# Optimization experiments

Hardware: AMD Instinct MI355X
Metric: run time of the kernel (lower is better)

The kernel has to match this reference:

```python
import jax, jax.numpy as jnp
import numpy as np

B, T, D = 16, 1024, 256   # batch, tokens, embedding_dim
Q, K = 4, 4096            # num_quantizers, n_embed
BETA = 1.0


def l2norm(x, eps=1e-12):
    n = jnp.linalg.norm(x, axis=-1, keepdims=True)
    return x / jnp.maximum(n, eps)


def vq_stage(z, codebook):
    """NormEMAVectorQuantizer forward (eval math; EMA buffer update omitted).
    z: (B,T,D) float; codebook: (K,D) l2-normalized rows.
    Returns straight-through quantized (B,T,D), scalar commit loss, indices (N,).
    """
    zn = l2norm(z)                                   # normalize input features
    zf = zn.reshape(-1, zn.shape[-1])                # (N, D)
    # squared euclidean distances (N, K): |z|^2 + |e|^2 - 2 z.e
    d = (jnp.sum(zf * zf, axis=1, keepdims=True)
         + jnp.sum(codebook * codebook, axis=1)[None, :]
         - 2.0 * zf @ codebook.T)
    idx = jnp.argmin(d, axis=1)                      # (N,)
    z_q = codebook[idx].reshape(zn.shape)            # gather codewords
    loss = BETA * jnp.mean((jax.lax.stop_gradient(z_q) - zn) ** 2)
    z_q = zn + jax.lax.stop_gradient(z_q - zn)       # straight-through
    return z_q, loss, idx


def setup_inputs() -> dict:
    key = jax.random.key(0)
    kx, kc = jax.random.split(key)
    x = jax.random.normal(kx, (B, T, D), dtype=jnp.float32)
    # EMA codebooks are kept l2-normalized in NormEMAVectorQuantizer
    codebooks = l2norm(jax.random.normal(kc, (Q, K, D), dtype=jnp.float32))
    return {"x": x, "codebooks": codebooks}


def reference(x, codebooks):
    residual = x
    quantized_outputs, losses, indices = [], [], []
    for q in range(codebooks.shape[0]):              # fixed small stage count
        z_q, loss, idx = vq_stage(residual, codebooks[q])
        # faithful to source: value of residual is unchanged, gradient path added
        residual = residual - jax.lax.stop_gradient(z_q) + z_q
        quantized_outputs.append(z_q)
        losses.append(loss)
        indices.append(idx)
    quantized_sum = quantized_outputs[0]
    for t in quantized_outputs[1:]:
        quantized_sum = quantized_sum + t
    total_loss = losses[0]
    for l in losses[1:]:
        total_loss = total_loss + l
    return quantized_sum, total_loss, jnp.stack(indices, axis=1)  # (N, Q) int
```

## Files before the change

### kernel.cpp

```cpp
#include <hip/hip_runtime.h>
#include <stdint.h>


#define NR 16384
#define DIM 256
#define KCB 4096
#define QST 4
#define MARGIN_DOT 4e-4f
#define MARGIN2_DOT 2e-5f
#define CAPL 4096

typedef _Float16 f16;
typedef __attribute__((ext_vector_type(4))) f16 f16x4;
typedef __attribute__((ext_vector_type(8))) f16 f16x8;
typedef __attribute__((ext_vector_type(4))) float f32x4;

#define WS_ZN_HI   ((size_t)0)
#define WS_ZN_LO   ((size_t)8*1024*1024)
#define WS_CB_HI   ((size_t)16*1024*1024)
#define WS_CB_LO   ((size_t)24*1024*1024)
#define WS_NORMS   ((size_t)32*1024*1024)
#define WS_SSQ     (WS_NORMS + 65536)
#define WS_TOPS    (WS_SSQ + 65536)
#define WS_IDX     (WS_TOPS + (size_t)QST*NR*2*16)
#define WS_LIST    (WS_IDX + (size_t)QST*NR*4)
#define WS_LIST2   (WS_LIST + (size_t)QST*CAPL*4)
#define WS_TOPS2   (WS_LIST2 + (size_t)QST*NR*4)
#define WS_CNT     (WS_TOPS2 + (size_t)QST*CAPL*16*16)
#define WS_PART    (WS_CNT + 64)
#define WS_TOPS3   (WS_PART + 16384)

__device__ __forceinline__ void gll16(const void* g, void* l) {
  __builtin_amdgcn_global_load_lds(
      (const __attribute__((address_space(1))) void*)g,
      (__attribute__((address_space(3))) void*)l, 16, 0, 0);
}

__device__ __forceinline__ float dot4chain(const float4* __restrict__ c,
                                           const float4* __restrict__ z) {
  float dot = 0.f;
  for (int d = 0; d < 64; ++d) {
    const float4 cv = c[d], zv = z[d];
    dot += cv.x * zv.x + cv.y * zv.y + cv.z * zv.z + cv.w * zv.w;
  }
  return dot;
}

__global__ void prep_kernel(const float* __restrict__ x, const float* __restrict__ cb,
                            char* __restrict__ ws) {
  const int w = threadIdx.x >> 6, lane = threadIdx.x & 63;
  const int normalize = (blockIdx.x < (NR / 4));
  const int blk = normalize ? blockIdx.x : blockIdx.x - (NR / 4);
  const float* src = normalize ? x : cb;
  const int row = blk * 4 + w;
  const float4 v = ((const float4*)src)[row * 64 + lane];
  float ss = v.x * v.x + v.y * v.y + v.z * v.z + v.w * v.w;
#pragma unroll
  for (int m = 32; m; m >>= 1) ss += __shfl_xor(ss, m);
  float4 z = v;
  f16 *hi, *lo;
  if (normalize) {
    const float denom = fmaxf(sqrtf(ss), 1e-12f);
    z.x = v.x / denom; z.y = v.y / denom; z.z = v.z / denom; z.w = v.w / denom;
    hi = (f16*)(ws + WS_ZN_HI); lo = (f16*)(ws + WS_ZN_LO);
    if (lane == 0) ((float*)(ws + WS_NORMS))[row] = denom;
    if (blockIdx.x == 0 && threadIdx.x < 8) ((int*)(ws + WS_CNT))[threadIdx.x] = 0;
  } else {
    hi = (f16*)(ws + WS_CB_HI); lo = (f16*)(ws + WS_CB_LO);
    if (lane == 0) ((float*)(ws + WS_SSQ))[row] = ss;
  }
  f16x4 h, l;
  h[0] = (f16)z.x; h[1] = (f16)z.y; h[2] = (f16)z.z; h[3] = (f16)z.w;
  l[0] = (f16)(z.x - (float)h[0]); l[1] = (f16)(z.y - (float)h[1]);
  l[2] = (f16)(z.z - (float)h[2]); l[3] = (f16)(z.w - (float)h[3]);
  ((f16x4*)hi)[row * 64 + lane] = h;
  ((f16x4*)lo)[row * 64 + lane] = l;
}

__launch_bounds__(256, 2)
__global__ void score_kernel(char* __restrict__ ws) {
  __shared__ __align__(16) f16 A0[128][64];
  __shared__ __align__(16) f16 A1[128][64];
  __shared__ __align__(16) f16 B0[128][64];
  __shared__ __align__(16) f16 B1[128][64];
  const int tid = threadIdx.x, w = tid >> 6, lane = tid & 63;
  const int wr = w >> 1, wc = w & 1;
  const int blk = blockIdx.x;
  const int xcd = blk & 7, st = xcd >> 1;
  const int rowtile = ((xcd & 1) << 6) + (blk >> 3);
  const int rowBase = rowtile << 7;

  const f16* zn_hi = (const f16*)(ws + WS_ZN_HI);
  const f16* cb_hi = (const f16*)(ws + WS_CB_HI);

  const int reg = w >> 1;
  const int half = w & 1;
  const int g0 = (lane & 7) ^ ((lane >> 3) & 7);
  const size_t laneOff = (size_t)(lane >> 3) * DIM + (size_t)g0 * 8;
  const f16* srcA0 = zn_hi + (size_t)(rowBase + half * 64) * DIM + laneOff;
  const f16* srcB0 = cb_hi + ((size_t)st * KCB + half * 64) * DIM + laneOff;

  f16* dst0 = reg ? &B0[half * 64][0] : &A0[half * 64][0];
  f16* dst1 = reg ? &B1[half * 64][0] : &A1[half * 64][0];

  float t1[16], t2[16]; int i1[16];
#pragma unroll
  for (int s = 0; s < 16; ++s) { t1[s] = -3.4e38f; t2[s] = -3.4e38f; i1[s] = 0; }
  const int colLane = wc * 64 + (lane & 15);

  auto SRC = [&](int ct, int dc) -> const f16* {
    return reg ? (srcB0 + (size_t)ct * 128 * DIM + dc * 64) : (srcA0 + dc * 64);
  };
  auto STAGE = [&](f16* dst, const f16* sp) {
#pragma unroll
    for (int op = 0; op < 8; ++op)
      gll16(sp + op * 8 * DIM, dst + op * 512);
  };

  f32x4 acc[4][4];
  const f32x4 zero4 = {0.f, 0.f, 0.f, 0.f};

  auto PHASE = [&](const f16* As, const f16* Bs, f16* stDst, const f16* stSrc,
                   bool doStage, bool init) {
    f16x8 ah[2][4], bh[2][4];
#pragma unroll
    for (int kk = 0; kk < 2; ++kk) {
#pragma unroll
      for (int m = 0; m < 4; ++m) {
        const int rl = wr * 64 + m * 16 + (lane & 15);
        const int slot = ((kk << 2) + (lane >> 4)) ^ (rl & 7);
        ah[kk][m] = *(const f16x8*)(As + rl * 64 + slot * 8);
      }
#pragma unroll
      for (int n = 0; n < 4; ++n) {
        const int cl = wc * 64 + n * 16 + (lane & 15);
        const int slot = ((kk << 2) + (lane >> 4)) ^ (cl & 7);
        bh[kk][n] = *(const f16x8*)(Bs + cl * 64 + slot * 8);
      }
    }
    if (doStage) STAGE(stDst, stSrc);
#pragma unroll
    for (int kk = 0; kk < 2; ++kk)
#pragma unroll
      for (int n = 0; n < 4; ++n) {
        if (init && kk == 0) {
#pragma unroll
          for (int m = 0; m < 4; ++m)
            acc[m][n] = __builtin_amdgcn_mfma_f32_16x16x32_f16(ah[0][m], bh[0][n], zero4, 0, 0, 0);
        } else {
#pragma unroll
          for (int m = 0; m < 4; ++m)
            acc[m][n] = __builtin_amdgcn_mfma_f32_16x16x32_f16(ah[kk][m], bh[kk][n], acc[m][n], 0, 0, 0);
        }
      }
    __syncthreads();
  };

  STAGE(dst0, SRC(0, 0));
  __syncthreads();

  for (int ct = 0; ct < 32; ++ct) {
    PHASE(&A0[0][0], &B0[0][0], dst1, SRC(ct, 1), true, true);
    PHASE(&A1[0][0], &B1[0][0], dst0, SRC(ct, 2), true, false);
    PHASE(&A0[0][0], &B0[0][0], dst1, SRC(ct, 3), true, false);
    PHASE(&A1[0][0], &B1[0][0], dst0, SRC(ct + 1, 0), ct < 31, false);
#pragma unroll
    for (int n = 0; n < 4; ++n) {
      const int col = ct * 128 + n * 16 + colLane;
#pragma unroll
      for (int m = 0; m < 4; ++m)
#pragma unroll
        for (int rr = 0; rr < 4; ++rr) {
          const float sc = acc[m][n][rr];
          const int sl = m * 4 + rr;
          if (sc > t1[sl]) { t2[sl] = t1[sl]; t1[sl] = sc; i1[sl] = col; }
          else t2[sl] = fmaxf(t2[sl], sc);
        }
    }
  }

  float* mv1 = (float*)&A0[0][0];
  float* mv2 = mv1 + 256;
  int*   mi1v = (int*)(mv2 + 256);
#pragma unroll
  for (int m = 0; m < 4; ++m)
#pragma unroll
    for (int rr = 0; rr < 4; ++rr) {
      const int sl = m * 4 + rr;
      float a1 = t1[sl], a2 = t2[sl]; int ai = i1[sl];
#pragma unroll
      for (int msk = 1; msk < 16; msk <<= 1) {
        const float o1 = __shfl_xor(a1, msk);
        const float o2 = __shfl_xor(a2, msk);
        const int   oi = __shfl_xor(ai, msk);
        if (o1 > a1)       { a2 = fmaxf(a1, o2); a1 = o1; ai = oi; }
        else if (o1 == a1) { a2 = a1; ai = min(ai, oi); }
        else               { a2 = fmaxf(a2, o1); }
      }
      if ((lane & 15) == 0) {
        const int rloc = wr * 64 + m * 16 + (lane >> 4) * 4 + rr;
        mv1[wc * 128 + rloc] = a1; mv2[wc * 128 + rloc] = a2; mi1v[wc * 128 + rloc] = ai;
      }
    }
  __syncthreads();
  if (tid < 128) {
    const float a1 = mv1[tid], a2 = mv2[tid]; const int ai = mi1v[tid];
    const float b1 = mv1[128 + tid], b2 = mv2[128 + tid]; const int bi = mi1v[128 + tid];
    float v1, v2; int fi;
    if (a1 > b1)      { v1 = a1; v2 = fmaxf(a2, b1); fi = ai; }
    else if (b1 > a1) { v1 = b1; v2 = fmaxf(b2, a1); fi = bi; }
    else { v1 = a1; v2 = a1; fi = min(ai, bi); }
    const int row = rowBase + tid;
    ((int*)(ws + WS_IDX))[row * 4 + st] = fi;
    if (v1 - v2 < MARGIN_DOT) {
      const int p = atomicAdd((int*)(ws + WS_CNT) + st, 1);
      if (p < CAPL) ((int*)(ws + WS_LIST))[st * CAPL + p] = row;
      else {
        const int p2 = atomicAdd((int*)(ws + WS_CNT) + 4 + st, 1);
        ((int*)(ws + WS_LIST2))[(size_t)st * NR + p2] = row;
      }
    }
  }
}

__launch_bounds__(256, 2)
__global__ void rescue_mfma_kernel(char* __restrict__ ws) {
  __shared__ __align__(16) f16 smem[4][128][64];
  __shared__ float mv1[2][128], mv2[2][128];
  __shared__ int   mi1[2][128];
  const int tid = threadIdx.x, w = tid >> 6, lane = tid & 63;
  const int wr = w >> 1, wc = w & 1;
  const int st = blockIdx.x & 3;
  const int kc = (blockIdx.x >> 2) & 15;
  const int slot = blockIdx.x >> 6;
  const int cnt = min(((const int*)(ws + WS_CNT))[st], CAPL);
  const int ntile = (cnt + 127) >> 7;
  const int* list = (const int*)(ws + WS_LIST) + st * CAPL;

  const f16* zn_hi = (const f16*)(ws + WS_ZN_HI);
  const f16* zn_lo = (const f16*)(ws + WS_ZN_LO);
  const f16* cb_hi = (const f16*)(ws + WS_CB_HI);
  const f16* cb_lo = (const f16*)(ws + WS_CB_LO);

  const int g0 = (lane & 7) ^ ((lane >> 3) & 7);
  const size_t laneOff = (size_t)(lane >> 3) * DIM + (size_t)g0 * 8;
  f16* ldsW = &smem[w][0][0];
  const f16* srcA = (w == 1) ? zn_lo : zn_hi;
  const f16* srcB = (w == 3) ? cb_lo : cb_hi;
  const int colLane = wc * 64 + (lane & 15);

  for (int tile = slot; tile < ntile; tile += 32) {
    const int base = tile << 7;
    int lid[16];
    if (w < 2) {
#pragma unroll
      for (int op = 0; op < 16; ++op) {
        const int i = base + op * 8 + (lane >> 3);
        lid[op] = list[min(i, cnt - 1)];
      }
    }
    float t1[16], t2[16]; int i1[16];
#pragma unroll
    for (int s = 0; s < 16; ++s) { t1[s] = -3.4e38f; t2[s] = -3.4e38f; i1[s] = 0; }

    for (int ct = kc * 2; ct < kc * 2 + 2; ++ct) {
      f32x4 acc[4][4];
#pragma unroll
      for (int m = 0; m < 4; ++m)
#pragma unroll
        for (int n = 0; n < 4; ++n) { acc[m][n][0] = 0.f; acc[m][n][1] = 0.f; acc[m][n][2] = 0.f; acc[m][n][3] = 0.f; }

      const f16* srcBBase = srcB + ((size_t)st * KCB + (size_t)ct * 128) * DIM + laneOff;

      for (int dc = 0; dc < 4; ++dc) {
        __syncthreads();
        if (w < 2) {
#pragma unroll
          for (int op = 0; op < 16; ++op)
            gll16(srcA + (size_t)lid[op] * DIM + dc * 64 + (size_t)g0 * 8,
                  ldsW + op * 512);
        } else {
          const f16* sp = srcBBase + dc * 64;
#pragma unroll
          for (int op = 0; op < 16; ++op)
            gll16(sp + op * 8 * DIM, ldsW + op * 512);
        }
        __syncthreads();

#pragma unroll
        for (int kk = 0; kk < 2; ++kk) {
          f16x8 ah[4], al[4];
#pragma unroll
          for (int m = 0; m < 4; ++m) {
            const int rl = wr * 64 + m * 16 + (lane & 15);
            const int slt = ((kk << 2) + (lane >> 4)) ^ (rl & 7);
            const int off = rl * 64 + slt * 8;
            ah[m] = *(const f16x8*)(&smem[0][0][0] + off);
            al[m] = *(const f16x8*)(&smem[1][0][0] + off);
          }
#pragma unroll
          for (int n = 0; n < 4; ++n) {
            const int cl = wc * 64 + n * 16 + (lane & 15);
            const int slt = ((kk << 2) + (lane >> 4)) ^ (cl & 7);
            const int off = cl * 64 + slt * 8;
            const f16x8 bh = *(const f16x8*)(&smem[2][0][0] + off);
            const f16x8 bl = *(const f16x8*)(&smem[3][0][0] + off);
#pragma unroll
            for (int m = 0; m < 4; ++m) {
              acc[m][n] = __builtin_amdgcn_mfma_f32_16x16x32_f16(ah[m], bh, acc[m][n], 0, 0, 0);
              acc[m][n] = __builtin_amdgcn_mfma_f32_16x16x32_f16(ah[m], bl, acc[m][n], 0, 0, 0);
              acc[m][n] = __builtin_amdgcn_mfma_f32_16x16x32_f16(al[m], bh, acc[m][n], 0, 0, 0);
            }
          }
        }
      }
#pragma unroll
      for (int n = 0; n < 4; ++n) {
        const int col = ct * 128 + n * 16 + colLane;
#pragma unroll
        for (int m = 0; m < 4; ++m)
#pragma unroll
          for (int r = 0; r < 4; ++r) {
            const float sc = acc[m][n][r];
            const int sl = m * 4 + r;
            if (sc > t1[sl]) { t2[sl] = t1[sl]; t1[sl] = sc; i1[sl] = col; }
            else t2[sl] = fmaxf(t2[sl], sc);
          }
      }
    }

#pragma unroll
    for (int m = 0; m < 4; ++m)
#pragma unroll
      for (int r = 0; r < 4; ++r) {
        const int sl = m * 4 + r;
        float a1 = t1[sl], a2 = t2[sl]; int ai = i1[sl];
#pragma unroll
        for (int msk = 1; msk < 16; msk <<= 1) {
          const float o1 = __shfl_xor(a1, msk);
          const float o2 = __shfl_xor(a2, msk);
          const int   oi = __shfl_xor(ai, msk);
          if (o1 > a1)       { a2 = fmaxf(a1, o2); a1 = o1; ai = oi; }
          else if (o1 == a1) { a2 = a1; ai = min(ai, oi); }
          else               { a2 = fmaxf(a2, o1); }
        }
        if ((lane & 15) == 0) {
          const int rloc = wr * 64 + m * 16 + (lane >> 4) * 4 + r;
          mv1[wc][rloc] = a1; mv2[wc][rloc] = a2; mi1[wc][rloc] = ai;
        }
      }
    __syncthreads();
    if (tid < 128 && base + tid < cnt) {
      const float a1 = mv1[0][tid], a2 = mv2[0][tid]; const int ai = mi1[0][tid];
      const float b1 = mv1[1][tid], b2 = mv2[1][tid]; const int bi = mi1[1][tid];
      float v1, v2; int fi;
      if (a1 > b1)      { v1 = a1; v2 = fmaxf(a2, b1); fi = ai; }
      else if (b1 > a1) { v1 = b1; v2 = fmaxf(b2, a1); fi = bi; }
      else { v1 = a1; v2 = a1; fi = min(ai, bi); }
      ((float4*)(ws + WS_TOPS2))[((size_t)(st * CAPL + base + tid) << 4) + kc] =
          make_float4(v1, v2, __int_as_float(fi), 0.f);
    }
    __syncthreads();
  }
}

__global__ void rescue_merge_kernel(char* __restrict__ ws) {
  const int t = blockIdx.x * 256 + threadIdx.x;
  const int st = t >> 12, j = t & (CAPL - 1);
  const int cnt = min(((const int*)(ws + WS_CNT))[st], CAPL);
  if (j >= cnt) return;
  const float4* p = (const float4*)(ws + WS_TOPS2) + ((size_t)(st * CAPL + j) << 4);
  float V1 = -3.4e38f, V2 = -3.4e38f; int I1 = 0;
#pragma unroll
  for (int c = 0; c < 16; ++c) {
    const float4 e = p[c];
    const float v1 = e.x, v2 = e.y; const int i1 = __float_as_int(e.z);
    if (v1 > V1) { V2 = fmaxf(V1, v2); V1 = v1; I1 = i1; }
    else {
      if (v1 == V1) I1 = min(I1, i1);
      V2 = fmaxf(V2, v1);
    }
  }
  const int row = ((const int*)(ws + WS_LIST))[st * CAPL + j];
  ((int*)(ws + WS_IDX))[row * 4 + st] = I1;
  if (V1 - V2 < MARGIN2_DOT) {
    const int p2 = atomicAdd((int*)(ws + WS_CNT) + 4 + st, 1);
    ((int*)(ws + WS_LIST2))[(size_t)st * NR + p2] = row;
  }
}

__global__ void rescue_exact_kernel(const float* __restrict__ x, const float* __restrict__ cb,
                                    char* __restrict__ ws) {
  __shared__ __align__(16) float zrow[DIM];
  __shared__ float zsq_s;
  __shared__ float lbv[4];
  __shared__ int   lbi[4];
  const int tid = threadIdx.x, w = tid >> 6, lane = tid & 63;
  const int st = blockIdx.x & 3;
  const int kc = (blockIdx.x >> 2) & 15;
  const int slot = blockIdx.x >> 6;
  const int cnt = min(((const int*)(ws + WS_CNT))[4 + st], CAPL);
  const int* list = (const int*)(ws + WS_LIST2) + (size_t)st * NR;
  const float* cbs = cb + (size_t)st * KCB * DIM;
  const float* ssqp = (const float*)(ws + WS_SSQ) + (size_t)st * KCB;
  int2* part = (int2*)(ws + WS_TOPS3);

  for (int j = slot; j < cnt; j += 16) {
    const int row = list[j];
    if (tid < 32) {
      const float denom = ((const float*)(ws + WS_NORMS))[row];
      const int g = tid;
      float ss = 0.f;
#pragma unroll
      for (int e = 0; e < 8; ++e) {
        const float v = x[(size_t)row * DIM + g * 8 + e] / denom;
        zrow[g * 8 + e] = v;
        ss += v * v;
      }
#pragma unroll
      for (int m = 16; m; m >>= 1) ss += __shfl_xor(ss, m);
      if (g == 0) zsq_s = ss;
    }
    __syncthreads();
    const float zsq = zsq_s;
    const int k = kc * 256 + tid;
    const float dot = dot4chain((const float4*)(cbs + (size_t)k * DIM), (const float4*)zrow);
    float bd = (zsq + ssqp[k]) - 2.0f * dot;
    int bi = k;
#pragma unroll
    for (int m = 32; m; m >>= 1) {
      const float od = __shfl_xor(bd, m);
      const int   oi = __shfl_xor(bi, m);
      if (od < bd || (od == bd && oi < bi)) { bd = od; bi = oi; }
    }
    if (lane == 0) { lbv[w] = bd; lbi[w] = bi; }
    __syncthreads();
    if (tid == 0) {
      float fb = lbv[0]; int fi = lbi[0];
#pragma unroll
      for (int ww = 1; ww < 4; ++ww)
        if (lbv[ww] < fb || (lbv[ww] == fb && lbi[ww] < fi)) { fb = lbv[ww]; fi = lbi[ww]; }
      part[((size_t)(st * CAPL + j) << 4) + kc] = make_int2(__float_as_int(fb), fi);
    }
    __syncthreads();
  }
}

__global__ void rescue_exact_merge_kernel(char* __restrict__ ws) {
  const int t = blockIdx.x * 256 + threadIdx.x;
  const int st = t >> 12, j = t & (CAPL - 1);
  const int cnt = min(((const int*)(ws + WS_CNT))[4 + st], CAPL);
  if (j >= cnt) return;
  const int2* part = (const int2*)(ws + WS_TOPS3) + ((size_t)(st * CAPL + j) << 4);
  float fb = 3.4e38f; int fi = 0x7fffffff;
#pragma unroll
  for (int kc = 0; kc < 16; ++kc) {
    const int2 e = part[kc];
    const float d = __int_as_float(e.x);
    if (d < fb || (d == fb && e.y < fi)) { fb = d; fi = e.y; }
  }
  const int row = ((const int*)(ws + WS_LIST2))[(size_t)st * NR + j];
  ((int*)(ws + WS_IDX))[row * 4 + st] = fi;
}

__global__ void rescue_tail_kernel(const float* __restrict__ x, const float* __restrict__ cb,
                                   char* __restrict__ ws) {
  __shared__ __align__(16) float zrows[8][DIM];
  __shared__ float zsqs[8];
  __shared__ float lbv[4][8];
  __shared__ int   lbi[4][8];
  const int tid = threadIdx.x, w = tid >> 6, lane = tid & 63;
  const int st = blockIdx.x & 3, slot = blockIdx.x >> 2;
  const int cnt = ((const int*)(ws + WS_CNT))[4 + st] - CAPL;
  if (cnt <= 0) return;
  const int nch = (cnt + 7) >> 3;
  const int* list = (const int*)(ws + WS_LIST2) + (size_t)st * NR + CAPL;
  const float* cbs = cb + (size_t)st * KCB * DIM;
  const float* ssqp = (const float*)(ws + WS_SSQ) + (size_t)st * KCB;

  for (int ch = slot; ch < nch; ch += 16) {
    const int base = ch * 8;
    const int nr = min(8, cnt - base);
    const int r = tid >> 5, g = tid & 31;
    if (r < nr) {
      const int row = list[base + r];
      const float denom = ((const float*)(ws + WS_NORMS))[row];
      float ss = 0.f;
#pragma unroll
      for (int j = 0; j < 8; ++j) {
        const float v = x[(size_t)row * DIM + g * 8 + j] / denom;
        zrows[r][g * 8 + j] = v;
        ss += v * v;
      }
#pragma unroll
      for (int m = 16; m; m >>= 1) ss += __shfl_xor(ss, m);
      if (g == 0) zsqs[r] = ss;
    }
    __syncthreads();

    float bd[8]; int bix[8];
#pragma unroll
    for (int q = 0; q < 8; ++q) { bd[q] = 3.4e38f; bix[q] = 0x7fffffff; }

    for (int k = tid; k < KCB; k += 256) {
      const float4* cr = (const float4*)(cbs + (size_t)k * DIM);
      const float4* zr = (const float4*)&zrows[0][0];
      float dot[8];
#pragma unroll
      for (int q = 0; q < 8; ++q) dot[q] = 0.f;
      for (int d = 0; d < 64; ++d) {
        const float4 cv = cr[d];
#pragma unroll
        for (int q = 0; q < 8; ++q) {
          const float4 zv = zr[q * 64 + d];
          dot[q] += cv.x * zv.x + cv.y * zv.y + cv.z * zv.z + cv.w * zv.w;
        }
      }
      const float sk = ssqp[k];
#pragma unroll
      for (int q = 0; q < 8; ++q) {
        const float dist = (zsqs[q] + sk) - 2.0f * dot[q];
        if (dist < bd[q]) { bd[q] = dist; bix[q] = k; }
      }
    }
#pragma unroll
    for (int q = 0; q < 8; ++q) {
#pragma unroll
      for (int m = 32; m; m >>= 1) {
        const float od = __shfl_xor(bd[q], m);
        const int   oi = __shfl_xor(bix[q], m);
        if (od < bd[q] || (od == bd[q] && oi < bix[q])) { bd[q] = od; bix[q] = oi; }
      }
      if (lane == 0) { lbv[w][q] = bd[q]; lbi[w][q] = bix[q]; }
    }
    __syncthreads();
    if (tid < 8 && tid < nr) {
      float fb = lbv[0][tid]; int fi = lbi[0][tid];
#pragma unroll
      for (int ww = 1; ww < 4; ++ww) {
        const float od = lbv[ww][tid]; const int oi = lbi[ww][tid];
        if (od < fb || (od == fb && oi < fi)) { fb = od; fi = oi; }
      }
      const int row = list[base + tid];
      ((int*)(ws + WS_IDX))[row * 4 + st] = fi;
    }
    __syncthreads();
  }
}

__global__ void finalize_kernel(const float* __restrict__ x, const float* __restrict__ cb,
                                char* __restrict__ ws, float* __restrict__ out) {
  __shared__ float wsum[4];
  const int w = threadIdx.x >> 6, lane = threadIdx.x & 63;
  const int row = blockIdx.x * 4 + w;
  const int* idxp = (const int*)(ws + WS_IDX) + (size_t)row * 4;
  const float denom = ((const float*)(ws + WS_NORMS))[row];
  const float4 xv = ((const float4*)x)[row * 64 + lane];
  const float4 zn = make_float4(xv.x / denom, xv.y / denom, xv.z / denom, xv.w / denom);
  float4 s = make_float4(0.f, 0.f, 0.f, 0.f);
  float lacc = 0.f;
#pragma unroll
  for (int q = 0; q < 4; ++q) {
    const int id = idxp[q];
    const float4 e = ((const float4*)(cb + ((size_t)q * KCB + id) * DIM))[lane];
    s.x += e.x; s.y += e.y; s.z += e.z; s.w += e.w;
    const float dx = e.x - zn.x, dy = e.y - zn.y, dz = e.z - zn.z, dw = e.w - zn.w;
    lacc += dx * dx + dy * dy + dz * dz + dw * dw;
  }
  ((float4*)out)[row * 64 + lane] = s;
  if (lane < 4) out[4194305 + (size_t)row * 4 + lane] = (float)idxp[lane];
#pragma unroll
  for (int m = 32; m; m >>= 1) lacc += __shfl_xor(lacc, m);
  if (lane == 0) wsum[w] = lacc;
  __syncthreads();
  if (threadIdx.x == 0)
    ((float*)(ws + WS_PART))[blockIdx.x] = wsum[0] + wsum[1] + wsum[2] + wsum[3];
}

__global__ void loss_final_kernel(const char* __restrict__ ws, float* __restrict__ out) {
  __shared__ float wsum[4];
  const int tid = threadIdx.x, w = tid >> 6, lane = tid & 63;
  const float* p = (const float*)(ws + WS_PART);
  float s = 0.f;
  for (int i = tid; i < 4096; i += 256) s += p[i];
#pragma unroll
  for (int m = 32; m; m >>= 1) s += __shfl_xor(s, m);
  if (lane == 0) wsum[w] = s;
  __syncthreads();
  if (tid == 0)
    out[4194304] = (wsum[0] + wsum[1] + wsum[2] + wsum[3]) * (1.0f / 4194304.0f);
}

extern "C" void kernel_launch(void* const* d_in, const int* in_sizes, int n_in,
                              void* d_out, int out_size, void* d_ws, size_t ws_size,
                              hipStream_t stream) {
  (void)in_sizes; (void)n_in; (void)out_size; (void)ws_size;
  const float* x = (const float*)d_in[0];
  const float* cb = (const float*)d_in[1];
  float* out = (float*)d_out;
  char* ws = (char*)d_ws;

  hipLaunchKernelGGL(prep_kernel, dim3(NR / 2), dim3(256), 0, stream, x, cb, ws);
  hipLaunchKernelGGL(score_kernel, dim3(512), dim3(256), 0, stream, ws);
  hipLaunchKernelGGL(rescue_mfma_kernel, dim3(2048), dim3(256), 0, stream, ws);
  hipLaunchKernelGGL(rescue_merge_kernel, dim3((QST * CAPL) / 256), dim3(256), 0, stream, ws);
  hipLaunchKernelGGL(rescue_exact_kernel, dim3(1024), dim3(256), 0, stream, x, cb, ws);
  hipLaunchKernelGGL(rescue_exact_merge_kernel, dim3((QST * CAPL) / 256), dim3(256), 0, stream, ws);
  hipLaunchKernelGGL(rescue_tail_kernel, dim3(64), dim3(256), 0, stream, x, cb, ws);
  hipLaunchKernelGGL(finalize_kernel, dim3(NR / 4), dim3(256), 0, stream, x, cb, ws, out);
  hipLaunchKernelGGL(loss_final_kernel, dim3(1), dim3(256), 0, stream, ws, out);
}
```

Before: 338.6 us.

## Keep A row tile resident in LDS and stream only codebook tiles

The score kernel now loads the full 128x256 A (normalized input) tile into LDS once, instead of restreaming it for every codebook column tile. Only the B codebook chunks are double-buffered, and all four waves share the staging, with each loading 32 rows per phase. This removes redundant global loads of A and halves per-phase staging work per wave. The cost is 96KB of LDS, so launch bounds drop to one block per CU, which lowers occupancy and latency hiding.

```diff
diff --git a/kernel.cpp b/kernel.cpp
--- a/kernel.cpp
+++ b/kernel.cpp
@@ -77,12 +77,14 @@
   ((f16x4*)lo)[row * 64 + lane] = l;
 }
 
-__launch_bounds__(256, 2)
+__launch_bounds__(256, 1)
 __global__ void score_kernel(char* __restrict__ ws) {
-  __shared__ __align__(16) f16 A0[128][64];
-  __shared__ __align__(16) f16 A1[128][64];
-  __shared__ __align__(16) f16 B0[128][64];
-  __shared__ __align__(16) f16 B1[128][64];
+  __shared__ __align__(16) f16 Astat0[128][64];
+  __shared__ __align__(16) f16 Astat1[128][64];
+  __shared__ __align__(16) f16 Astat2[128][64];
+  __shared__ __align__(16) f16 Astat3[128][64];
+  __shared__ __align__(16) f16 Bb0[128][64];
+  __shared__ __align__(16) f16 Bb1[128][64];
   const int tid = threadIdx.x, w = tid >> 6, lane = tid & 63;
   const int wr = w >> 1, wc = w & 1;
   const int blk = blockIdx.x;
@@ -99,26 +101,40 @@
   const size_t laneOff = (size_t)(lane >> 3) * DIM + (size_t)g0 * 8;
   const f16* srcA0 = zn_hi + (size_t)(rowBase + half * 64) * DIM + laneOff;
   const f16* srcB0 = cb_hi + ((size_t)st * KCB + half * 64) * DIM + laneOff;
-
-  f16* dst0 = reg ? &B0[half * 64][0] : &A0[half * 64][0];
-  f16* dst1 = reg ? &B1[half * 64][0] : &A1[half * 64][0];
+  const f16* srcBq0 = cb_hi + ((size_t)st * KCB + w * 32) * DIM + laneOff;
 
   float t1[16], t2[16]; int i1[16];
 #pragma unroll
   for (int s = 0; s < 16; ++s) { t1[s] = -3.4e38f; t2[s] = -3.4e38f; i1[s] = 0; }
   const int colLane = wc * 64 + (lane & 15);
 
-  auto SRC = [&](int ct, int dc) -> const f16* {
-    return reg ? (srcB0 + (size_t)ct * 128 * DIM + dc * 64) : (srcA0 + dc * 64);
-  };
-  auto STAGE = [&](f16* dst, const f16* sp) {
+  if (reg == 0) {
+#pragma unroll
+    for (int dc = 0; dc < 4; ++dc) {
+      f16* ad = (dc == 0) ? &Astat0[half * 64][0]
+              : (dc == 1) ? &Astat1[half * 64][0]
+              : (dc == 2) ? &Astat2[half * 64][0]
+                          : &Astat3[half * 64][0];
+      const f16* sp = srcA0 + dc * 64;
+#pragma unroll
+      for (int op = 0; op < 8; ++op)
+        gll16(sp + op * 8 * DIM, ad + op * 512);
+    }
+  } else {
 #pragma unroll
     for (int op = 0; op < 8; ++op)
+      gll16(srcB0 + op * 8 * DIM, &Bb0[half * 64][0] + op * 512);
+  }
+  __syncthreads();
+
+  f32x4 acc[4][4];
+  const f32x4 zero4 = {0.f, 0.f, 0.f, 0.f};
+
+  auto STAGE4 = [&](f16* dst, const f16* sp) {
+#pragma unroll
+    for (int op = 0; op < 4; ++op)
       gll16(sp + op * 8 * DIM, dst + op * 512);
   };
-
-  f32x4 acc[4][4];
-  const f32x4 zero4 = {0.f, 0.f, 0.f, 0.f};
 
   auto PHASE = [&](const f16* As, const f16* Bs, f16* stDst, const f16* stSrc,
                    bool doStage, bool init) {
@@ -138,7 +154,7 @@
         bh[kk][n] = *(const f16x8*)(Bs + cl * 64 + slot * 8);
       }
     }
-    if (doStage) STAGE(stDst, stSrc);
+    if (doStage) STAGE4(stDst, stSrc);
 #pragma unroll
     for (int kk = 0; kk < 2; ++kk)
 #pragma unroll
@@ -156,14 +172,12 @@
     __syncthreads();
   };
 
-  STAGE(dst0, SRC(0, 0));
-  __syncthreads();
-
   for (int ct = 0; ct < 32; ++ct) {
-    PHASE(&A0[0][0], &B0[0][0], dst1, SRC(ct, 1), true, true);
-    PHASE(&A1[0][0], &B1[0][0], dst0, SRC(ct, 2), true, false);
-    PHASE(&A0[0][0], &B0[0][0], dst1, SRC(ct, 3), true, false);
-    PHASE(&A1[0][0], &B1[0][0], dst0, SRC(ct + 1, 0), ct < 31, false);
+    const f16* sB = srcBq0 + (size_t)ct * 128 * DIM;
+    PHASE(&Astat0[0][0], &Bb0[0][0], &Bb1[w * 32][0], sB + 1 * 64, true, true);
+    PHASE(&Astat1[0][0], &Bb1[0][0], &Bb0[w * 32][0], sB + 2 * 64, true, false);
+    PHASE(&Astat2[0][0], &Bb0[0][0], &Bb1[w * 32][0], sB + 3 * 64, true, false);
+    PHASE(&Astat3[0][0], &Bb1[0][0], &Bb0[w * 32][0], sB + (size_t)128 * DIM, ct < 31, false);
 #pragma unroll
     for (int n = 0; n < 4; ++n) {
       const int col = ct * 128 + n * 16 + colLane;
@@ -179,7 +193,7 @@
     }
   }
 
-  float* mv1 = (float*)&A0[0][0];
+  float* mv1 = (float*)&Astat0[0][0];
   float* mv2 = mv1 + 256;
   int*   mi1v = (int*)(mv2 + 256);
 #pragma unroll
```

Result: slower. 392.9 us (+16.0%).
